# Kernel tuning notes

Measured on AMD Instinct MI355X. Metric: run time of the kernel, lower is better.

## Reference

```python
import jax, jax.numpy as jnp
import numpy as np

EPS = 1e-5  # torch BatchNorm1d default eps


def _project(x, w1, gamma, beta, w2):
    # Linear(bias=False) -> BatchNorm1d (train mode: batch stats, biased var) -> ReLU -> Linear(bias=False)
    h = x @ w1                                   # (n, 128)
    mu = jnp.mean(h, axis=0)
    var = jnp.var(h, axis=0)                     # biased, as torch uses for normalization
    h = (h - mu) * jax.lax.rsqrt(var + EPS) * gamma + beta
    h = jax.nn.relu(h)
    return h @ w2                                # (n, 128)


def setup_inputs() -> dict:
    key = jax.random.key(0)
    k1, k2, k3, k4 = jax.random.split(key, 4)
    latent, hidden = 512, 128
    n_x, n_y = 8192, 2048
    return {
        "variations": jax.random.normal(k1, (n_x, latent), dtype=jnp.float32),
        "exemplar": jax.random.normal(k2, (n_y, latent), dtype=jnp.float32),
        "w1": jax.random.normal(k3, (latent, hidden), dtype=jnp.float32) * (1.0 / np.sqrt(latent)),
        "gamma": jnp.ones((hidden,), dtype=jnp.float32),
        "beta": jnp.zeros((hidden,), dtype=jnp.float32),
        "w2": jax.random.normal(k4, (hidden, hidden), dtype=jnp.float32) * (1.0 / np.sqrt(hidden)),
    }


def reference(variations, exemplar, w1, gamma, beta, w2):
    z1 = _project(variations, w1, gamma, beta, w2)   # (n_x, d)
    z2 = _project(exemplar, w1, gamma, beta, w2)     # (n_y, d)
    # avoids the (n_x, n_y, d) broadcast intermediate of the original)
    x2 = jnp.sum(z1 * z1, axis=1)[:, None]           # (n_x, 1)
    y2 = jnp.sum(z2 * z2, axis=1)[None, :]           # (1, n_y)
    return x2 + y2 - 2.0 * (z1 @ z2.T)               # (n_x, n_y)
```

## Files before the change

### kernel.cpp

```cpp
#include <hip/hip_runtime.h>
#include <hip/hip_bf16.h>


#define LAT 512
#define HID 128
#define EPSV 1e-5f

typedef __attribute__((ext_vector_type(8))) short bf16x8;
typedef __attribute__((ext_vector_type(4))) float f32x4;

__device__ __forceinline__ unsigned short f2bf(float x) {
  unsigned int u = __builtin_bit_cast(unsigned int, x);
  return (unsigned short)((u + 0x7fffu + ((u >> 16) & 1u)) >> 16);
}
__device__ __forceinline__ float bf2f(unsigned short h) {
  unsigned int u = ((unsigned int)h) << 16;
  return __builtin_bit_cast(float, u);
}
__device__ __forceinline__ size_t pack4_off(int strip, int f, int l15, int lq) {
  return (size_t)strip * 2048 + (size_t)(f >> 1) * 512 + (size_t)l15 * 32 +
         (size_t)(((f & 1) * 2 + (lq >> 1)) * 8 + (lq & 1) * 4);
}

__global__ __launch_bounds__(256) void k_prep(const float* __restrict__ W1,
                                              const float* __restrict__ W2,
                                              const float* __restrict__ X1,
                                              const float* __restrict__ X2, int nx,
                                              unsigned short* __restrict__ W1P,
                                              unsigned short* __restrict__ W2T,
                                              unsigned short* __restrict__ XbP) {
  __shared__ float T[64][65];
  const int t = threadIdx.x;
  int bi = blockIdx.x;
  if (bi >= 20) {
    const size_t base = (size_t)(bi - 20) * 2048 + (size_t)t * 8;
    const size_t nxe = (size_t)nx * LAT;
    const float* src = (base < nxe) ? (X1 + base) : (X2 + (base - nxe));
    const float4 a = *(const float4*)src;
    const float4 b = *(const float4*)(src + 4);
    const int row = (int)(base >> 9);
    const int k = (int)(base & 511);
    const int st = row >> 4, l15 = row & 15;
    const int tf = k >> 5, lq = (k >> 3) & 3;
    const size_t off = ((((size_t)st * 16 + tf) * 16 + l15) * 4 + lq) * 8;
    const ushort4 o0 = {f2bf(a.x), f2bf(a.y), f2bf(a.z), f2bf(a.w)};
    const ushort4 o1 = {f2bf(b.x), f2bf(b.y), f2bf(b.z), f2bf(b.w)};
    *(ushort4*)(XbP + off) = o0;
    *(ushort4*)(XbP + off + 4) = o1;
    return;
  }
  if (bi < 16) {
    const int tk = bi >> 1, tn = bi & 1;
    const int k0 = tk * 64, n0 = tn * 64;
    {
      const int rr = t >> 4, cc = (t & 15) * 4;
#pragma unroll
      for (int i = 0; i < 4; ++i) {
        const int r = rr + i * 16;
        const float4 v = *(const float4*)(W1 + (size_t)(k0 + r) * HID + n0 + cc);
        T[cc + 0][r] = v.x; T[cc + 1][r] = v.y; T[cc + 2][r] = v.z; T[cc + 3][r] = v.w;
      }
    }
    __syncthreads();
    {
      const int nn = t >> 2, q = (t & 3) * 16;
      const int n = n0 + nn;
      const int f = n >> 4, l15 = n & 15;
#pragma unroll
      for (int e8 = 0; e8 < 2; ++e8) {
        const int kq = q + e8 * 8;
        const int kk = k0 + kq;
        const int tf = kk >> 5, lq = (kk >> 3) & 3;
        const size_t off = ((((size_t)f * 16 + tf) * 16 + l15) * 4 + lq) * 8;
        const ushort4 lo = {f2bf(T[nn][kq + 0]), f2bf(T[nn][kq + 1]),
                            f2bf(T[nn][kq + 2]), f2bf(T[nn][kq + 3])};
        const ushort4 hi = {f2bf(T[nn][kq + 4]), f2bf(T[nn][kq + 5]),
                            f2bf(T[nn][kq + 6]), f2bf(T[nn][kq + 7])};
        *(ushort4*)(W1P + off) = lo;
        *(ushort4*)(W1P + off + 4) = hi;
      }
    }
  } else {
    bi -= 16;
    const int tk = bi >> 1, tn = bi & 1;
    const int k0 = tk * 64, n0 = tn * 64;
    {
      const int rr = t >> 4, cc = (t & 15) * 4;
#pragma unroll
      for (int i = 0; i < 4; ++i) {
        const int r = rr + i * 16;
        const float4 v = *(const float4*)(W2 + (size_t)(k0 + r) * HID + n0 + cc);
        T[cc + 0][r] = v.x; T[cc + 1][r] = v.y; T[cc + 2][r] = v.z; T[cc + 3][r] = v.w;
      }
    }
    __syncthreads();
    {
      const int nn = t >> 2, q = (t & 3) * 16;
      unsigned short* dp = W2T + (size_t)(n0 + nn) * HID + k0 + q;
#pragma unroll
      for (int j = 0; j < 4; ++j) {
        ushort4 o = {f2bf(T[nn][q + j * 4 + 0]), f2bf(T[nn][q + j * 4 + 1]),
                     f2bf(T[nn][q + j * 4 + 2]), f2bf(T[nn][q + j * 4 + 3])};
        *(ushort4*)(dp + j * 4) = o;
      }
    }
  }
}

__global__ __launch_bounds__(256, 1) void k_gemm1(
    const unsigned short* __restrict__ XbP,
    const unsigned short* __restrict__ W1P, unsigned short* __restrict__ H,
    float* __restrict__ pS, float* __restrict__ pQ) {
  __shared__ float sS[16][HID], sQ[16][HID];
  const int tid = threadIdx.x, wid = tid >> 6, lane = tid & 63;
  const int l15 = lane & 15, lq = lane >> 4;
  const int row0 = (int)blockIdx.x * 64 + wid * 16;
  const int strip = row0 >> 4;
  const unsigned short* xp = XbP + (size_t)strip * 8192 + (size_t)l15 * 32 + lq * 8;
  const unsigned short* wp = W1P + (size_t)l15 * 32 + lq * 8;
  f32x4 acc[8];
#pragma unroll
  for (int f = 0; f < 8; ++f) acc[f] = (f32x4){0.f, 0.f, 0.f, 0.f};

  bf16x8 xb[4];
  bf16x8 ab[4][8];
#pragma unroll
  for (int p = 0; p < 4; ++p) {
    xb[p] = *(const bf16x8*)(xp + (size_t)p * 512);
#pragma unroll
    for (int f = 0; f < 8; ++f)
      ab[p][f] = *(const bf16x8*)(wp + (size_t)(f * 16 + p) * 512);
  }
#pragma unroll
  for (int t = 0; t < 16; ++t) {
    const int s = t & 3;
#pragma unroll
    for (int f = 0; f < 8; ++f) {
      acc[f] = __builtin_amdgcn_mfma_f32_16x16x32_bf16(ab[s][f], xb[s], acc[f], 0, 0, 0);
      if (t + 4 < 16)
        ab[s][f] = *(const bf16x8*)(wp + (size_t)(f * 16 + t + 4) * 512);
    }
    if (t + 4 < 16) xb[s] = *(const bf16x8*)(xp + (size_t)(t + 4) * 512);
  }
#pragma unroll
  for (int f = 0; f < 8; ++f) {
    ushort4 hz = {f2bf(acc[f][0]), f2bf(acc[f][1]), f2bf(acc[f][2]), f2bf(acc[f][3])};
    *(ushort4*)(H + pack4_off(strip, f, l15, lq)) = hz;
  }
#pragma unroll
  for (int f = 0; f < 8; ++f) {
    f32x4 s = acc[f];
    f32x4 q = acc[f] * acc[f];
#pragma unroll
    for (int r = 0; r < 4; ++r) {
      s[r] += __shfl_xor(s[r], 1, 64);
      q[r] += __shfl_xor(q[r], 1, 64);
      s[r] += __shfl_xor(s[r], 2, 64);
      q[r] += __shfl_xor(q[r], 2, 64);
    }
    if ((l15 & 3) == 0) {
      *(f32x4*)&sS[wid * 4 + (l15 >> 2)][f * 16 + lq * 4] = s;
      *(f32x4*)&sQ[wid * 4 + (l15 >> 2)][f * 16 + lq * 4] = q;
    }
  }
  __syncthreads();
  if (tid < HID) {
    float s = 0.f, q = 0.f;
#pragma unroll
    for (int r = 0; r < 16; ++r) { s += sS[r][tid]; q += sQ[r][tid]; }
    pS[(size_t)blockIdx.x * HID + tid] = s;
    pQ[(size_t)blockIdx.x * HID + tid] = q;
  }
}

__global__ __launch_bounds__(256) void k_gemm2(
    const unsigned short* __restrict__ H,
    const unsigned short* __restrict__ W2T,
    const float* __restrict__ pS, const float* __restrict__ pQ,
    const float* __restrict__ gamma, const float* __restrict__ beta,
    unsigned short* __restrict__ Z, float* __restrict__ nrm,
    int nb1, int nblk, float n1c, float n2c) {
  __shared__ float s_sc[HID], s_sh[HID];
  __shared__ float t0[2][HID], t1[2][HID];
  const int tid = threadIdx.x, wid = tid >> 6, lane = tid & 63;
  const int l15 = lane & 15, lq = lane >> 4, lk8 = lq * 8;
  const bool set1 = (int)blockIdx.x < nb1;
  {
    const int col = tid & 127, half = tid >> 7;
    const int b0 = set1 ? 0 : nb1;
    const int nb = set1 ? nb1 : (nblk - nb1);
    float s = 0.f, q = 0.f;
#pragma unroll 4
    for (int b = half; b < nb; b += 2) {
      s += pS[(size_t)(b0 + b) * HID + col];
      q += pQ[(size_t)(b0 + b) * HID + col];
    }
    t0[half][col] = s;
    t1[half][col] = q;
  }
  __syncthreads();
  if (tid < HID) {
    const float s = t0[0][tid] + t0[1][tid];
    const float q = t1[0][tid] + t1[1][tid];
    const float n = set1 ? n1c : n2c;
    const float mean = s / n;
    const float var = q / n - mean * mean;
    const float rstd = rsqrtf(var + EPSV);
    const float scale = gamma[tid] * rstd;
    s_sc[tid] = scale;
    s_sh[tid] = beta[tid] - mean * scale;
  }
  __syncthreads();
  const int row0 = (int)blockIdx.x * 64 + wid * 16;
  const int strip = row0 >> 4;
  const unsigned short* hptr = H + (size_t)strip * 2048 + (size_t)l15 * 32 + lk8;
  f32x4 acc[8];
#pragma unroll
  for (int f = 0; f < 8; ++f) acc[f] = (f32x4){0.f, 0.f, 0.f, 0.f};
#pragma unroll
  for (int s = 0; s < 4; ++s) {
    const int k = s * 32 + lk8;
    const bf16x8 hv = *(const bf16x8*)(hptr + (size_t)s * 512);
    const float4 c0 = *(const float4*)&s_sc[k];
    const float4 c1 = *(const float4*)&s_sc[k + 4];
    const float4 d0 = *(const float4*)&s_sh[k];
    const float4 d1 = *(const float4*)&s_sh[k + 4];
    const float cc[8] = {c0.x, c0.y, c0.z, c0.w, c1.x, c1.y, c1.z, c1.w};
    const float dd[8] = {d0.x, d0.y, d0.z, d0.w, d1.x, d1.y, d1.z, d1.w};
    bf16x8 bfr;
#pragma unroll
    for (int i = 0; i < 8; ++i) {
      const float a = fmaxf(fmaf(bf2f((unsigned short)hv[i]), cc[i], dd[i]), 0.f);
      bfr[i] = (short)f2bf(a);
    }
#pragma unroll
    for (int f = 0; f < 8; ++f) {
      const bf16x8 afr = *(const bf16x8*)(W2T + (size_t)(f * 16 + l15) * HID + k);
      acc[f] = __builtin_amdgcn_mfma_f32_16x16x32_bf16(afr, bfr, acc[f], 0, 0, 0);
    }
  }
  float rn = 0.f;
#pragma unroll
  for (int f = 0; f < 8; ++f) {
    rn += acc[f][0] * acc[f][0] + acc[f][1] * acc[f][1] +
          acc[f][2] * acc[f][2] + acc[f][3] * acc[f][3];
    ushort4 z4 = {f2bf(acc[f][0]), f2bf(acc[f][1]), f2bf(acc[f][2]), f2bf(acc[f][3])};
    *(ushort4*)(Z + pack4_off(strip, f, l15, lq)) = z4;
  }
  rn += __shfl_xor(rn, 16, 64);
  rn += __shfl_xor(rn, 32, 64);
  if (lane < 16) nrm[row0 + l15] = rn;
}

__global__ __launch_bounds__(256) void k_dist(const unsigned short* __restrict__ Z1b,
                                              const unsigned short* __restrict__ Z2b,
                                              const float* __restrict__ n1,
                                              const float* __restrict__ n2,
                                              float* __restrict__ D, int NY, int ntx) {
  const int nwg = (int)gridDim.x;
  const int cpx = nwg >> 3;
  const int bid = (int)blockIdx.x;
  const int wgid = (bid & 7) * cpx + (bid >> 3);
  const int tby = wgid / ntx, tbx = wgid - tby * ntx;

  const int tid = threadIdx.x;
  const int wid = tid >> 6, lane = tid & 63;
  const int wr = wid >> 1, wc = wid & 1;
  const int rowB = tby * 128 + wr * 64;
  const int colB = tbx * 128 + wc * 64;
  const int l15 = lane & 15, lq = lane >> 4;
  const unsigned short* Ap = Z1b + (size_t)(rowB >> 4) * 2048 + (size_t)l15 * 32 + lq * 8;
  const unsigned short* Bp = Z2b + (size_t)(colB >> 4) * 2048 + (size_t)l15 * 32 + lq * 8;
  f32x4 acc[4][4];
#pragma unroll
  for (int i = 0; i < 4; ++i)
#pragma unroll
    for (int j = 0; j < 4; ++j) acc[i][j] = (f32x4){0.f, 0.f, 0.f, 0.f};
#pragma unroll
  for (int s = 0; s < 4; ++s) {
    bf16x8 a[4], b[4];
#pragma unroll
    for (int i = 0; i < 4; ++i) a[i] = *(const bf16x8*)(Ap + (size_t)i * 2048 + (size_t)s * 512);
#pragma unroll
    for (int j = 0; j < 4; ++j) b[j] = *(const bf16x8*)(Bp + (size_t)j * 2048 + (size_t)s * 512);
#pragma unroll
    for (int i = 0; i < 4; ++i)
#pragma unroll
      for (int j = 0; j < 4; ++j)
        acc[i][j] = __builtin_amdgcn_mfma_f32_16x16x32_bf16(b[j], a[i], acc[i][j], 0, 0, 0);
  }
  const int cq = lq * 4;
  float na[4];
#pragma unroll
  for (int i = 0; i < 4; ++i) na[i] = n1[rowB + i * 16 + l15];
#pragma unroll
  for (int j = 0; j < 4; ++j) {
    const float4 nbv = *(const float4*)(n2 + colB + j * 16 + cq);
#pragma unroll
    for (int i = 0; i < 4; ++i) {
      float4 o;
      o.x = na[i] + nbv.x - 2.f * acc[i][j][0];
      o.y = na[i] + nbv.y - 2.f * acc[i][j][1];
      o.z = na[i] + nbv.z - 2.f * acc[i][j][2];
      o.w = na[i] + nbv.w - 2.f * acc[i][j][3];
      *(float4*)(D + (size_t)(rowB + i * 16 + l15) * NY + colB + j * 16 + cq) = o;
    }
  }
}

extern "C" void kernel_launch(void* const* d_in, const int* in_sizes, int n_in,
                              void* d_out, int out_size, void* d_ws, size_t ws_size,
                              hipStream_t stream) {
  const float* variations = (const float*)d_in[0];
  const float* exemplar   = (const float*)d_in[1];
  const float* w1         = (const float*)d_in[2];
  const float* gamma      = (const float*)d_in[3];
  const float* beta       = (const float*)d_in[4];
  const float* w2         = (const float*)d_in[5];
  float* D = (float*)d_out;

  const int nx = in_sizes[0] / LAT;
  const int ny = in_sizes[1] / LAT;
  const int nrows = nx + ny;
  const int nbb = nrows / 64;
  const int nb1 = nx / 64;

  char* p = (char*)d_ws;
  unsigned short* XbP = (unsigned short*)p; p += (size_t)nrows * LAT * 2;
  unsigned short* Hb  = (unsigned short*)p; p += (size_t)nrows * HID * 2;
  unsigned short* Zb  = (unsigned short*)p; p += (size_t)nrows * HID * 2;
  unsigned short* W1P = (unsigned short*)p; p += (size_t)LAT * HID * 2;
  unsigned short* W2T = (unsigned short*)p; p += (size_t)HID * HID * 2;
  float* pS = (float*)p;  p += (size_t)nbb * HID * 4;
  float* pQ = (float*)p;  p += (size_t)nbb * HID * 4;
  float* nrmAll = (float*)p; p += (size_t)nrows * 4;
  float* n1v = nrmAll;
  float* n2v = nrmAll + nx;
  unsigned short* Z1b = Zb;
  unsigned short* Z2b = Zb + (size_t)nx * HID;

  const int xblocks = (nrows * LAT) / 2048;
  k_prep<<<20 + xblocks, 256, 0, stream>>>(w1, w2, variations, exemplar, nx,
                                           W1P, W2T, XbP);
  k_gemm1<<<nbb, 256, 0, stream>>>(XbP, W1P, Hb, pS, pQ);
  k_gemm2<<<nbb, 256, 0, stream>>>(Hb, W2T, pS, pQ, gamma, beta, Zb, nrmAll,
                                   nb1, nbb, (float)nx, (float)ny);
  const int ntx = ny / 128;
  const int nwg = (nx / 128) * ntx;
  k_dist<<<nwg, 256, 0, stream>>>(Z1b, Z2b, n1v, n2v, D, ny, ntx);
}
```

Baseline: 57.26 us.

## Fuse fp32-to-bf16 input conversion into first GEMM, drop packed X buffer

```diff
diff --git a/kernel.cpp b/kernel.cpp
--- a/kernel.cpp
+++ b/kernel.cpp
@@ -24,31 +24,11 @@
 
 __global__ __launch_bounds__(256) void k_prep(const float* __restrict__ W1,
                                               const float* __restrict__ W2,
-                                              const float* __restrict__ X1,
-                                              const float* __restrict__ X2, int nx,
                                               unsigned short* __restrict__ W1P,
-                                              unsigned short* __restrict__ W2T,
-                                              unsigned short* __restrict__ XbP) {
+                                              unsigned short* __restrict__ W2T) {
   __shared__ float T[64][65];
   const int t = threadIdx.x;
   int bi = blockIdx.x;
-  if (bi >= 20) {
-    const size_t base = (size_t)(bi - 20) * 2048 + (size_t)t * 8;
-    const size_t nxe = (size_t)nx * LAT;
-    const float* src = (base < nxe) ? (X1 + base) : (X2 + (base - nxe));
-    const float4 a = *(const float4*)src;
-    const float4 b = *(const float4*)(src + 4);
-    const int row = (int)(base >> 9);
-    const int k = (int)(base & 511);
-    const int st = row >> 4, l15 = row & 15;
-    const int tf = k >> 5, lq = (k >> 3) & 3;
-    const size_t off = ((((size_t)st * 16 + tf) * 16 + l15) * 4 + lq) * 8;
-    const ushort4 o0 = {f2bf(a.x), f2bf(a.y), f2bf(a.z), f2bf(a.w)};
-    const ushort4 o1 = {f2bf(b.x), f2bf(b.y), f2bf(b.z), f2bf(b.w)};
-    *(ushort4*)(XbP + off) = o0;
-    *(ushort4*)(XbP + off + 4) = o1;
-    return;
-  }
   if (bi < 16) {
     const int tk = bi >> 1, tn = bi & 1;
     const int k0 = tk * 64, n0 = tn * 64;
@@ -108,25 +88,29 @@
 }
 
 __global__ __launch_bounds__(256, 1) void k_gemm1(
-    const unsigned short* __restrict__ XbP,
+    const float* __restrict__ X1, const float* __restrict__ X2, int nx,
     const unsigned short* __restrict__ W1P, unsigned short* __restrict__ H,
     float* __restrict__ pS, float* __restrict__ pQ) {
   __shared__ float sS[16][HID], sQ[16][HID];
   const int tid = threadIdx.x, wid = tid >> 6, lane = tid & 63;
   const int l15 = lane & 15, lq = lane >> 4;
-  const int row0 = (int)blockIdx.x * 64 + wid * 16;
+  const int browBase = (int)blockIdx.x * 64;
+  const int row0 = browBase + wid * 16;
   const int strip = row0 >> 4;
-  const unsigned short* xp = XbP + (size_t)strip * 8192 + (size_t)l15 * 32 + lq * 8;
+  const float* X = (browBase < nx) ? X1 : X2;
+  const int xrow = (browBase < nx) ? row0 : row0 - nx;
+  const float* xptr = X + (size_t)(xrow + l15) * LAT + lq * 8;
   const unsigned short* wp = W1P + (size_t)l15 * 32 + lq * 8;
   f32x4 acc[8];
 #pragma unroll
   for (int f = 0; f < 8; ++f) acc[f] = (f32x4){0.f, 0.f, 0.f, 0.f};
 
-  bf16x8 xb[4];
+  float4 xa[4], xb4[4];
   bf16x8 ab[4][8];
 #pragma unroll
   for (int p = 0; p < 4; ++p) {
-    xb[p] = *(const bf16x8*)(xp + (size_t)p * 512);
+    xa[p] = *(const float4*)(xptr + p * 32);
+    xb4[p] = *(const float4*)(xptr + p * 32 + 4);
 #pragma unroll
     for (int f = 0; f < 8; ++f)
       ab[p][f] = *(const bf16x8*)(wp + (size_t)(f * 16 + p) * 512);
@@ -134,13 +118,21 @@
 #pragma unroll
   for (int t = 0; t < 16; ++t) {
     const int s = t & 3;
+    const float vv[8] = {xa[s].x, xa[s].y, xa[s].z, xa[s].w,
+                         xb4[s].x, xb4[s].y, xb4[s].z, xb4[s].w};
+    bf16x8 xv;
+#pragma unroll
+    for (int i = 0; i < 8; ++i) xv[i] = (short)f2bf(vv[i]);
+    if (t + 4 < 16) {
+      xa[s] = *(const float4*)(xptr + (t + 4) * 32);
+      xb4[s] = *(const float4*)(xptr + (t + 4) * 32 + 4);
+    }
 #pragma unroll
     for (int f = 0; f < 8; ++f) {
-      acc[f] = __builtin_amdgcn_mfma_f32_16x16x32_bf16(ab[s][f], xb[s], acc[f], 0, 0, 0);
+      acc[f] = __builtin_amdgcn_mfma_f32_16x16x32_bf16(ab[s][f], xv, acc[f], 0, 0, 0);
       if (t + 4 < 16)
         ab[s][f] = *(const bf16x8*)(wp + (size_t)(f * 16 + t + 4) * 512);
     }
-    if (t + 4 < 16) xb[s] = *(const bf16x8*)(xp + (size_t)(t + 4) * 512);
   }
 #pragma unroll
   for (int f = 0; f < 8; ++f) {
@@ -326,7 +318,6 @@
   const int nb1 = nx / 64;
 
   char* p = (char*)d_ws;
-  unsigned short* XbP = (unsigned short*)p; p += (size_t)nrows * LAT * 2;
   unsigned short* Hb  = (unsigned short*)p; p += (size_t)nrows * HID * 2;
   unsigned short* Zb  = (unsigned short*)p; p += (size_t)nrows * HID * 2;
   unsigned short* W1P = (unsigned short*)p; p += (size_t)LAT * HID * 2;
@@ -339,10 +330,8 @@
   unsigned short* Z1b = Zb;
   unsigned short* Z2b = Zb + (size_t)nx * HID;
 
-  const int xblocks = (nrows * LAT) / 2048;
-  k_prep<<<20 + xblocks, 256, 0, stream>>>(w1, w2, variations, exemplar, nx,
-                                           W1P, W2T, XbP);
-  k_gemm1<<<nbb, 256, 0, stream>>>(XbP, W1P, Hb, pS, pQ);
+  k_prep<<<20, 256, 0, stream>>>(w1, w2, W1P, W2T);
+  k_gemm1<<<nbb, 256, 0, stream>>>(variations, exemplar, nx, W1P, Hb, pS, pQ);
   k_gemm2<<<nbb, 256, 0, stream>>>(Hb, W2T, pS, pQ, gamma, beta, Zb, nrmAll,
                                    nb1, nbb, (float)nx, (float)ny);
   const int ntx = ny / 128;
```

New measurement: 57.29 us (median of 2 runs). No clear change (+0.1%).
